# Kernel optimization log

Measured on AMD Instinct MI355X. Metric: run time of the kernel, lower is better.

## Reference

```python
import math
import jax, jax.numpy as jnp
import numpy as np

DIM = 128
NUM_PROJ = 256
B, H, SEQ = 2, 16, 4096


def _make_orthogonal_S(key):
    # Mirrors QJLWithOrthogonal.__init__: raw Gaussian, QR-orthogonalize each
    # dim-row chunk, scale by sqrt(dim).
    raw = jax.random.normal(key, (NUM_PROJ, DIM), dtype=jnp.float32)
    blocks = []
    for start in range(0, NUM_PROJ, DIM):
        block = raw[start:min(start + DIM, NUM_PROJ)]
        if block.shape[0] <= block.shape[1]:
            q, _ = jnp.linalg.qr(block.T)  # reduced QR of [dim, rows]
            blocks.append(q.T * np.float32(math.sqrt(DIM)))
        else:
            blocks.append(block)
    return jnp.concatenate(blocks, axis=0)[:NUM_PROJ]


def setup_inputs() -> dict:
    key = jax.random.key(0)
    kq, kk, ks = jax.random.split(key, 3)
    query = jax.random.normal(kq, (B, H, SEQ, DIM), dtype=jnp.float32)
    key_t = jax.random.normal(kk, (B, H, SEQ, DIM), dtype=jnp.float32)
    S = _make_orthogonal_S(ks)
    return {"query": query, "key": key_t, "S": S}


def reference(query, key, S):
    # quantize(key): sign of JL projection -> {-1, +1}, shape [B,H,S,m]
    z = jnp.sign(jnp.einsum('bhsd,md->bhsm', key, S))
    # estimate_inner_product(query, z): asymmetric estimator
    qp = jnp.einsum('bhsd,md->bhsm', query, S)
    scale = np.float32(math.sqrt(math.pi / 2) / NUM_PROJ)
    return scale * jnp.sum(qp * z, axis=-1)  # [B,H,S]
```

## Files before the change

kernel.cpp:

```cpp
#include <hip/hip_runtime.h>
#include <hip/hip_bf16.h>


#define DIM        128
#define NPROJ      256
#define TILE_T     32
#define NWG        4096
#define NBLK_P     256
#define TILES_PB   (NWG / NBLK_P)
#define LDS_STRIDE 136
#define TAU        6.0e-3f
#define SCALE      0.0048957583489668f

#define SHI_ELEMS  32768
#define TILE_ELEMS (TILE_T * LDS_STRIDE)
#define SMEM_BYTES ((2*SHI_ELEMS + 3*TILE_ELEMS) * 2 + 4 * TILE_T * 4)

typedef __attribute__((ext_vector_type(8))) short short8;
typedef __attribute__((ext_vector_type(4))) float f32x4;

static __device__ __forceinline__ unsigned short bf16_rne(float x){
    unsigned int u = __builtin_bit_cast(unsigned int, x);
    u += 0x7FFFu + ((u >> 16) & 1u);
    return (unsigned short)(u >> 16);
}

static __device__ __attribute__((noinline))
float ref_sign(const float* __restrict__ Kg, const float* __restrict__ S,
               int tok, int m){
    const float4* kr = (const float4*)(Kg + (size_t)tok * DIM);
    const float4* sr = (const float4*)(S  + (size_t)m   * DIM);
    float acc = 0.f;
#pragma unroll 4
    for (int d = 0; d < DIM/4; ++d){
        float4 k4 = kr[d];
        float4 s4 = sr[d];
        acc = __builtin_fmaf(k4.x, s4.x, acc);
        acc = __builtin_fmaf(k4.y, s4.y, acc);
        acc = __builtin_fmaf(k4.z, s4.z, acc);
        acc = __builtin_fmaf(k4.w, s4.w, acc);
    }
    return (acc > 0.f) ? 1.f : ((acc < 0.f) ? -1.f : 0.f);
}

__global__ void prep_s_kernel(const float* __restrict__ S,
                              unsigned short* __restrict__ shi,
                              unsigned short* __restrict__ slo){
    int t    = blockIdx.x * 256 + threadIdx.x;
    int lane = t & 63;
    int ms   = (t >> 6) & 3;
    int ks   = (t >> 8) & 3;
    int g    = (t >> 10) & 3;
    int m    = g*64 + ms*16 + (lane & 15);
    int d    = ks*32 + (lane >> 4)*8;
    const float4* p = (const float4*)(S + (size_t)m*DIM + d);
    float4 x0 = p[0], x1 = p[1];
    float xs[8] = {x0.x,x0.y,x0.z,x0.w, x1.x,x1.y,x1.z,x1.w};
    size_t base = ((size_t)t) * 8;
    unsigned long long h0=0,h1=0,l0=0,l1=0;
#pragma unroll
    for (int e = 0; e < 4; ++e){
        unsigned short hb = bf16_rne(xs[e]);
        float hf = __builtin_bit_cast(float, (unsigned int)hb << 16);
        h0 |= (unsigned long long)hb                    << (16*e);
        l0 |= (unsigned long long)bf16_rne(xs[e] - hf)  << (16*e);
    }
#pragma unroll
    for (int e = 0; e < 4; ++e){
        unsigned short hb = bf16_rne(xs[4+e]);
        float hf = __builtin_bit_cast(float, (unsigned int)hb << 16);
        h1 |= (unsigned long long)hb                      << (16*e);
        l1 |= (unsigned long long)bf16_rne(xs[4+e] - hf)  << (16*e);
    }
    *(unsigned long long*)(shi + base)     = h0;
    *(unsigned long long*)(shi + base + 4) = h1;
    *(unsigned long long*)(slo + base)     = l0;
    *(unsigned long long*)(slo + base + 4) = l1;
}


__global__ __launch_bounds__(256, 1)
void qjl_persistent(const float* __restrict__ Qg, const float* __restrict__ Kg,
                    const float* __restrict__ S,
                    const unsigned short* __restrict__ shi_tab,
                    const unsigned short* __restrict__ slo_tab,
                    float* __restrict__ out)
{
    extern __shared__ unsigned short smem_us[];
    unsigned short* s_hi = smem_us;
    unsigned short* s_lo = s_hi + SHI_ELEMS;
    unsigned short* khi  = s_lo + SHI_ELEMS;
    unsigned short* klo  = khi + TILE_ELEMS;
    unsigned short* qhi  = klo + TILE_ELEMS;
    float* red = (float*)(qhi + TILE_ELEMS);

    const int tid  = threadIdx.x;
    const int wave = tid >> 6;
    const int lane = tid & 63;
    const int l16  = lane & 15;
    const int quad = lane >> 4;

    {
        const short8* gh = (const short8*)shi_tab;
        const short8* gl = (const short8*)slo_tab;
        short8* lh = (short8*)s_hi;
        short8* ll = (short8*)s_lo;
#pragma unroll
        for (int j = 0; j < 16; ++j){
            int c = tid + j*256;
            lh[c] = gh[c];
            ll[c] = gl[c];
        }
    }

    float4 kv[4], qv[4];
    {
        const size_t t0 = (size_t)blockIdx.x * TILES_PB * TILE_T * DIM;
        const float4* ksrc = (const float4*)(Kg + t0);
        const float4* qsrc = (const float4*)(Qg + t0);
#pragma unroll
        for (int j = 0; j < 4; ++j){ kv[j] = ksrc[tid + j*256]; qv[j] = qsrc[tid + j*256]; }
    }

#pragma unroll 1
    for (int it = 0; it < TILES_PB; ++it){
        const int tok0 = (blockIdx.x * TILES_PB + it) * TILE_T;

#pragma unroll
        for (int j = 0; j < 4; ++j){
            int i   = tid + j*256;
            int row = i >> 5;
            int c   = i & 31;
            float kx[4] = {kv[j].x, kv[j].y, kv[j].z, kv[j].w};
            float qx[4] = {qv[j].x, qv[j].y, qv[j].z, qv[j].w};
            unsigned long long hp = 0, lp = 0, qp = 0;
#pragma unroll
            for (int e = 0; e < 4; ++e){
                unsigned short hb = bf16_rne(kx[e]);
                float hf = __builtin_bit_cast(float, (unsigned int)hb << 16);
                hp |= (unsigned long long)hb                   << (16*e);
                lp |= (unsigned long long)bf16_rne(kx[e] - hf) << (16*e);
                qp |= (unsigned long long)bf16_rne(qx[e])      << (16*e);
            }
            int base = row * LDS_STRIDE + c*4;
            *(unsigned long long*)(khi + base) = hp;
            *(unsigned long long*)(klo + base) = lp;
            *(unsigned long long*)(qhi + base) = qp;
        }
        __syncthreads();

        if (it + 1 < TILES_PB){
            const size_t tn = (size_t)(tok0 + TILE_T) * DIM;
            const float4* ksrc = (const float4*)(Kg + tn);
            const float4* qsrc = (const float4*)(Qg + tn);
#pragma unroll
            for (int j = 0; j < 4; ++j){ kv[j] = ksrc[tid + j*256]; qv[j] = qsrc[tid + j*256]; }
        }

        f32x4 accC[4][2];
        f32x4 accQ[4][2];
#pragma unroll
        for (int ms = 0; ms < 4; ++ms)
#pragma unroll
            for (int ts = 0; ts < 2; ++ts){
                accC[ms][ts] = (f32x4){0.f,0.f,0.f,0.f};
                accQ[ms][ts] = (f32x4){0.f,0.f,0.f,0.f};
            }

#pragma unroll
        for (int ks = 0; ks < 4; ++ks){
            short8 ah[4], al[4];
#pragma unroll
            for (int ms = 0; ms < 4; ++ms){
                int off = (((wave*4 + ks)*4 + ms)*64 + lane)*8;
                ah[ms] = *(const short8*)(s_hi + off);
                al[ms] = *(const short8*)(s_lo + off);
            }
#pragma unroll
            for (int ts = 0; ts < 2; ++ts){
                const int off = (ts*16 + l16) * LDS_STRIDE + ks*32 + quad*8;
                short8 bk = *(const short8*)(khi + off);
                short8 bl = *(const short8*)(klo + off);
                short8 bq = *(const short8*)(qhi + off);
#pragma unroll
                for (int ms = 0; ms < 4; ++ms){
                    accC[ms][ts] = __builtin_amdgcn_mfma_f32_16x16x32_bf16(ah[ms], bk, accC[ms][ts], 0,0,0);
                    accC[ms][ts] = __builtin_amdgcn_mfma_f32_16x16x32_bf16(al[ms], bk, accC[ms][ts], 0,0,0);
                    accC[ms][ts] = __builtin_amdgcn_mfma_f32_16x16x32_bf16(ah[ms], bl, accC[ms][ts], 0,0,0);
                    accQ[ms][ts] = __builtin_amdgcn_mfma_f32_16x16x32_bf16(ah[ms], bq, accQ[ms][ts], 0,0,0);
                }
            }
        }

        float part0 = 0.f, part1 = 0.f;
#pragma unroll
        for (int ts = 0; ts < 2; ++ts){
#pragma unroll
            for (int ms = 0; ms < 4; ++ms){
#pragma unroll
                for (int r = 0; r < 4; ++r){
                    float c = accC[ms][ts][r];
                    float s = (c >= 0.f) ? 1.f : -1.f;
                    if (__builtin_fabsf(c) < TAU)
                        s = ref_sign(Kg, S, tok0 + ts*16 + l16,
                                     wave*64 + ms*16 + quad*4 + r);
                    float sv = s * accQ[ms][ts][r];
                    if (ts) part1 += sv; else part0 += sv;
                }
            }
        }

        part0 += __shfl_xor(part0, 16, 64);
        part0 += __shfl_xor(part0, 32, 64);
        part1 += __shfl_xor(part1, 16, 64);
        part1 += __shfl_xor(part1, 32, 64);
        if (quad == 0){
            red[wave*TILE_T + l16]      = part0;
            red[wave*TILE_T + 16 + l16] = part1;
        }
        __syncthreads();
        if (tid < TILE_T)
            out[tok0 + tid] = SCALE * (red[0*TILE_T + tid] + red[1*TILE_T + tid] +
                                       red[2*TILE_T + tid] + red[3*TILE_T + tid]);
    }
}


template<bool USE_TAB>
static __device__ __forceinline__
void load_afrags(const unsigned short* __restrict__ shi_tab,
                 const unsigned short* __restrict__ slo_tab,
                 const float* __restrict__ S,
                 int wave, int ks, int l16, int quad, int lane,
                 short8 ah[4], short8 al[4]){
    if (USE_TAB){
#pragma unroll
        for (int ms = 0; ms < 4; ++ms){
            size_t off = ((size_t)((wave*4 + ks)*4 + ms)*64 + lane)*8;
            ah[ms] = *(const short8*)(shi_tab + off);
            al[ms] = *(const short8*)(slo_tab + off);
        }
    } else {
#pragma unroll
        for (int ms = 0; ms < 4; ++ms){
            const float4* p = (const float4*)(S + (size_t)(wave*64 + ms*16 + l16)*DIM
                                              + ks*32 + quad*8);
            float4 x0 = p[0], x1 = p[1];
            float xs[8] = {x0.x,x0.y,x0.z,x0.w, x1.x,x1.y,x1.z,x1.w};
            short8 h, l;
#pragma unroll
            for (int e = 0; e < 8; ++e){
                unsigned short hb = bf16_rne(xs[e]);
                float hf = __builtin_bit_cast(float, (unsigned int)hb << 16);
                h[e] = (short)hb;
                l[e] = (short)bf16_rne(xs[e] - hf);
            }
            ah[ms] = h;
            al[ms] = l;
        }
    }
}

template<bool USE_TAB>
__global__ __launch_bounds__(256, 4)
void qjl_kernel(const float* __restrict__ Qg, const float* __restrict__ Kg,
                const float* __restrict__ S,
                const unsigned short* __restrict__ shi_tab,
                const unsigned short* __restrict__ slo_tab,
                float* __restrict__ out)
{
    __shared__ unsigned short khi[TILE_T * LDS_STRIDE];
    __shared__ unsigned short klo[TILE_T * LDS_STRIDE];
    __shared__ unsigned short qhi[TILE_T * LDS_STRIDE];
    __shared__ float red[4][TILE_T];

    const int tid  = threadIdx.x;
    const int wave = tid >> 6;
    const int lane = tid & 63;
    const int l16  = lane & 15;
    const int quad = lane >> 4;
    const int tok0 = blockIdx.x * TILE_T;

    {
        const float4* ksrc = (const float4*)(Kg + (size_t)tok0 * DIM);
        const float4* qsrc = (const float4*)(Qg + (size_t)tok0 * DIM);
        float4 kv[4], qv[4];
#pragma unroll
        for (int j = 0; j < 4; ++j){ kv[j] = ksrc[tid + j*256]; qv[j] = qsrc[tid + j*256]; }
#pragma unroll
        for (int j = 0; j < 4; ++j){
            int i   = tid + j*256;
            int row = i >> 5;
            int c   = i & 31;
            float kx[4] = {kv[j].x, kv[j].y, kv[j].z, kv[j].w};
            float qx[4] = {qv[j].x, qv[j].y, qv[j].z, qv[j].w};
            unsigned long long hp = 0, lp = 0, qp = 0;
#pragma unroll
            for (int e = 0; e < 4; ++e){
                unsigned short hb = bf16_rne(kx[e]);
                float hf = __builtin_bit_cast(float, (unsigned int)hb << 16);
                hp |= (unsigned long long)hb                   << (16*e);
                lp |= (unsigned long long)bf16_rne(kx[e] - hf) << (16*e);
                qp |= (unsigned long long)bf16_rne(qx[e])      << (16*e);
            }
            int base = row * LDS_STRIDE + c*4;
            *(unsigned long long*)(khi + base) = hp;
            *(unsigned long long*)(klo + base) = lp;
            *(unsigned long long*)(qhi + base) = qp;
        }
    }
    __syncthreads();

    f32x4 accC[4][2];
    f32x4 accQ[4][2];
#pragma unroll
    for (int ms = 0; ms < 4; ++ms)
#pragma unroll
        for (int ts = 0; ts < 2; ++ts){
            accC[ms][ts] = (f32x4){0.f,0.f,0.f,0.f};
            accQ[ms][ts] = (f32x4){0.f,0.f,0.f,0.f};
        }

#pragma unroll
    for (int ks = 0; ks < 4; ++ks){
        short8 ah[4], al[4];
        load_afrags<USE_TAB>(shi_tab, slo_tab, S, wave, ks, l16, quad, lane, ah, al);
#pragma unroll
        for (int ts = 0; ts < 2; ++ts){
            const int off = (ts*16 + l16) * LDS_STRIDE + ks*32 + quad*8;
            short8 bk = *(const short8*)(khi + off);
            short8 bl = *(const short8*)(klo + off);
            short8 bq = *(const short8*)(qhi + off);
#pragma unroll
            for (int ms = 0; ms < 4; ++ms){
                accC[ms][ts] = __builtin_amdgcn_mfma_f32_16x16x32_bf16(ah[ms], bk, accC[ms][ts], 0,0,0);
                accC[ms][ts] = __builtin_amdgcn_mfma_f32_16x16x32_bf16(al[ms], bk, accC[ms][ts], 0,0,0);
                accC[ms][ts] = __builtin_amdgcn_mfma_f32_16x16x32_bf16(ah[ms], bl, accC[ms][ts], 0,0,0);
                accQ[ms][ts] = __builtin_amdgcn_mfma_f32_16x16x32_bf16(ah[ms], bq, accQ[ms][ts], 0,0,0);
            }
        }
    }

    float part0 = 0.f, part1 = 0.f;
#pragma unroll
    for (int ts = 0; ts < 2; ++ts){
#pragma unroll
        for (int ms = 0; ms < 4; ++ms){
#pragma unroll
            for (int r = 0; r < 4; ++r){
                float c = accC[ms][ts][r];
                float s = (c >= 0.f) ? 1.f : -1.f;
                if (__builtin_fabsf(c) < TAU)
                    s = ref_sign(Kg, S, tok0 + ts*16 + l16,
                                 wave*64 + ms*16 + quad*4 + r);
                float sv = s * accQ[ms][ts][r];
                if (ts) part1 += sv; else part0 += sv;
            }
        }
    }

    part0 += __shfl_xor(part0, 16, 64);
    part0 += __shfl_xor(part0, 32, 64);
    part1 += __shfl_xor(part1, 16, 64);
    part1 += __shfl_xor(part1, 32, 64);
    if (quad == 0){
        red[wave][l16]      = part0;
        red[wave][16 + l16] = part1;
    }
    __syncthreads();
    if (tid < TILE_T)
        out[tok0 + tid] = SCALE * (red[0][tid] + red[1][tid] + red[2][tid] + red[3][tid]);
}

extern "C" void kernel_launch(void* const* d_in, const int* in_sizes, int n_in,
                              void* d_out, int out_size, void* d_ws, size_t ws_size,
                              hipStream_t stream){
    const float* Qg = (const float*)d_in[0];
    const float* Kg = (const float*)d_in[1];
    const float* S  = (const float*)d_in[2];
    float* out = (float*)d_out;

    const size_t tab_elems = (size_t)NPROJ * DIM;
    const size_t need = 2 * tab_elems * sizeof(unsigned short);

    static int attr_ok = -1;
    if (attr_ok < 0){
        hipError_t e = hipFuncSetAttribute(
            reinterpret_cast<const void*>(&qjl_persistent),
            hipFuncAttributeMaxDynamicSharedMemorySize, SMEM_BYTES);
        attr_ok = (e == hipSuccess) ? 1 : 0;
    }

    if (d_ws && ws_size >= need){
        unsigned short* shi = (unsigned short*)d_ws;
        unsigned short* slo = shi + tab_elems;
        prep_s_kernel<<<16, 256, 0, stream>>>(S, shi, slo);
        if (attr_ok){
            qjl_persistent<<<NBLK_P, 256, SMEM_BYTES, stream>>>(Qg, Kg, S, shi, slo, out);
        } else {
            qjl_kernel<true><<<NWG, 256, 0, stream>>>(Qg, Kg, S, shi, slo, out);
        }
    } else {
        qjl_kernel<false><<<NWG, 256, 0, stream>>>(Qg, Kg, S, nullptr, nullptr, out);
    }
}
```

Measured before the change: 223.1 us.

## Hold projection fragments in registers and launch more smaller blocks

The persistent kernel staged the full bf16 hi/lo projection tables in about 140KB of LDS, allowing only one block per CU. The new kernel loads each wave's slice of the tables into registers once (32 short8 fragments per lane), keeps only the token tiles in LDS, and launches 1024 blocks of 4 tiles with a two-blocks-per-CU launch bound. The MFMA calls are also regrouped by operand so independent accumulators are issued back to back. This removes the per-iteration LDS reads of the A fragments and raises occupancy, at the cost of heavy VGPR pressure (128 registers for fragments) and a per-block table reload from global/L2.

```diff
diff --git a/kernel.cpp b/kernel.cpp
--- a/kernel.cpp
+++ b/kernel.cpp
@@ -6,15 +6,11 @@
 #define NPROJ      256
 #define TILE_T     32
 #define NWG        4096
-#define NBLK_P     256
-#define TILES_PB   (NWG / NBLK_P)
+#define NBLK_R     1024
+#define TPB        4
 #define LDS_STRIDE 136
 #define TAU        6.0e-3f
 #define SCALE      0.0048957583489668f
-
-#define SHI_ELEMS  32768
-#define TILE_ELEMS (TILE_T * LDS_STRIDE)
-#define SMEM_BYTES ((2*SHI_ELEMS + 3*TILE_ELEMS) * 2 + 4 * TILE_T * 4)
 
 typedef __attribute__((ext_vector_type(8))) short short8;
 typedef __attribute__((ext_vector_type(4))) float f32x4;
@@ -79,20 +75,17 @@
 }
 
 
-__global__ __launch_bounds__(256, 1)
-void qjl_persistent(const float* __restrict__ Qg, const float* __restrict__ Kg,
-                    const float* __restrict__ S,
-                    const unsigned short* __restrict__ shi_tab,
-                    const unsigned short* __restrict__ slo_tab,
-                    float* __restrict__ out)
+__global__ __launch_bounds__(256, 2)
+void qjl_reg(const float* __restrict__ Qg, const float* __restrict__ Kg,
+             const float* __restrict__ S,
+             const unsigned short* __restrict__ shi_tab,
+             const unsigned short* __restrict__ slo_tab,
+             float* __restrict__ out)
 {
-    extern __shared__ unsigned short smem_us[];
-    unsigned short* s_hi = smem_us;
-    unsigned short* s_lo = s_hi + SHI_ELEMS;
-    unsigned short* khi  = s_lo + SHI_ELEMS;
-    unsigned short* klo  = khi + TILE_ELEMS;
-    unsigned short* qhi  = klo + TILE_ELEMS;
-    float* red = (float*)(qhi + TILE_ELEMS);
+    __shared__ unsigned short khi[TILE_T * LDS_STRIDE];
+    __shared__ unsigned short klo[TILE_T * LDS_STRIDE];
+    __shared__ unsigned short qhi[TILE_T * LDS_STRIDE];
+    __shared__ float red[4][TILE_T];
 
     const int tid  = threadIdx.x;
     const int wave = tid >> 6;
@@ -100,22 +93,19 @@
     const int l16  = lane & 15;
     const int quad = lane >> 4;
 
-    {
-        const short8* gh = (const short8*)shi_tab;
-        const short8* gl = (const short8*)slo_tab;
-        short8* lh = (short8*)s_hi;
-        short8* ll = (short8*)s_lo;
-#pragma unroll
-        for (int j = 0; j < 16; ++j){
-            int c = tid + j*256;
-            lh[c] = gh[c];
-            ll[c] = gl[c];
-        }
-    }
+    short8 sh[4][4], sl[4][4];
+#pragma unroll
+    for (int ks = 0; ks < 4; ++ks)
+#pragma unroll
+        for (int ms = 0; ms < 4; ++ms){
+            size_t off = ((size_t)((wave*4 + ks)*4 + ms)*64 + lane)*8;
+            sh[ks][ms] = *(const short8*)(shi_tab + off);
+            sl[ks][ms] = *(const short8*)(slo_tab + off);
+        }
 
     float4 kv[4], qv[4];
     {
-        const size_t t0 = (size_t)blockIdx.x * TILES_PB * TILE_T * DIM;
+        const size_t t0 = (size_t)blockIdx.x * TPB * TILE_T * DIM;
         const float4* ksrc = (const float4*)(Kg + t0);
         const float4* qsrc = (const float4*)(Qg + t0);
 #pragma unroll
@@ -123,8 +113,8 @@
     }
 
 #pragma unroll 1
-    for (int it = 0; it < TILES_PB; ++it){
-        const int tok0 = (blockIdx.x * TILES_PB + it) * TILE_T;
+    for (int it = 0; it < TPB; ++it){
+        const int tok0 = (blockIdx.x * TPB + it) * TILE_T;
 
 #pragma unroll
         for (int j = 0; j < 4; ++j){
@@ -149,7 +139,7 @@
         }
         __syncthreads();
 
-        if (it + 1 < TILES_PB){
+        if (it + 1 < TPB){
             const size_t tn = (size_t)(tok0 + TILE_T) * DIM;
             const float4* ksrc = (const float4*)(Kg + tn);
             const float4* qsrc = (const float4*)(Qg + tn);
@@ -169,13 +159,6 @@
 
 #pragma unroll
         for (int ks = 0; ks < 4; ++ks){
-            short8 ah[4], al[4];
-#pragma unroll
-            for (int ms = 0; ms < 4; ++ms){
-                int off = (((wave*4 + ks)*4 + ms)*64 + lane)*8;
-                ah[ms] = *(const short8*)(s_hi + off);
-                al[ms] = *(const short8*)(s_lo + off);
-            }
 #pragma unroll
             for (int ts = 0; ts < 2; ++ts){
                 const int off = (ts*16 + l16) * LDS_STRIDE + ks*32 + quad*8;
@@ -183,12 +166,17 @@
                 short8 bl = *(const short8*)(klo + off);
                 short8 bq = *(const short8*)(qhi + off);
 #pragma unroll
-                for (int ms = 0; ms < 4; ++ms){
-                    accC[ms][ts] = __builtin_amdgcn_mfma_f32_16x16x32_bf16(ah[ms], bk, accC[ms][ts], 0,0,0);
-                    accC[ms][ts] = __builtin_amdgcn_mfma_f32_16x16x32_bf16(al[ms], bk, accC[ms][ts], 0,0,0);
-                    accC[ms][ts] = __builtin_amdgcn_mfma_f32_16x16x32_bf16(ah[ms], bl, accC[ms][ts], 0,0,0);
-                    accQ[ms][ts] = __builtin_amdgcn_mfma_f32_16x16x32_bf16(ah[ms], bq, accQ[ms][ts], 0,0,0);
-                }
+                for (int ms = 0; ms < 4; ++ms)
+                    accC[ms][ts] = __builtin_amdgcn_mfma_f32_16x16x32_bf16(sh[ks][ms], bk, accC[ms][ts], 0,0,0);
+#pragma unroll
+                for (int ms = 0; ms < 4; ++ms)
+                    accC[ms][ts] = __builtin_amdgcn_mfma_f32_16x16x32_bf16(sl[ks][ms], bk, accC[ms][ts], 0,0,0);
+#pragma unroll
+                for (int ms = 0; ms < 4; ++ms)
+                    accC[ms][ts] = __builtin_amdgcn_mfma_f32_16x16x32_bf16(sh[ks][ms], bl, accC[ms][ts], 0,0,0);
+#pragma unroll
+                for (int ms = 0; ms < 4; ++ms)
+                    accQ[ms][ts] = __builtin_amdgcn_mfma_f32_16x16x32_bf16(sh[ks][ms], bq, accQ[ms][ts], 0,0,0);
             }
         }
 
@@ -215,13 +203,12 @@
         part1 += __shfl_xor(part1, 16, 64);
         part1 += __shfl_xor(part1, 32, 64);
         if (quad == 0){
-            red[wave*TILE_T + l16]      = part0;
-            red[wave*TILE_T + 16 + l16] = part1;
+            red[wave][l16]      = part0;
+            red[wave][16 + l16] = part1;
         }
         __syncthreads();
         if (tid < TILE_T)
-            out[tok0 + tid] = SCALE * (red[0*TILE_T + tid] + red[1*TILE_T + tid] +
-                                       red[2*TILE_T + tid] + red[3*TILE_T + tid]);
+            out[tok0 + tid] = SCALE * (red[0][tid] + red[1][tid] + red[2][tid] + red[3][tid]);
     }
 }
 
@@ -383,23 +370,11 @@
     const size_t tab_elems = (size_t)NPROJ * DIM;
     const size_t need = 2 * tab_elems * sizeof(unsigned short);
 
-    static int attr_ok = -1;
-    if (attr_ok < 0){
-        hipError_t e = hipFuncSetAttribute(
-            reinterpret_cast<const void*>(&qjl_persistent),
-            hipFuncAttributeMaxDynamicSharedMemorySize, SMEM_BYTES);
-        attr_ok = (e == hipSuccess) ? 1 : 0;
-    }
-
     if (d_ws && ws_size >= need){
         unsigned short* shi = (unsigned short*)d_ws;
         unsigned short* slo = shi + tab_elems;
         prep_s_kernel<<<16, 256, 0, stream>>>(S, shi, slo);
-        if (attr_ok){
-            qjl_persistent<<<NBLK_P, 256, SMEM_BYTES, stream>>>(Qg, Kg, S, shi, slo, out);
-        } else {
-            qjl_kernel<true><<<NWG, 256, 0, stream>>>(Qg, Kg, S, shi, slo, out);
-        }
+        qjl_reg<<<NBLK_R, 256, 0, stream>>>(Qg, Kg, S, shi, slo, out);
     } else {
         qjl_kernel<false><<<NWG, 256, 0, stream>>>(Qg, Kg, S, nullptr, nullptr, out);
     }
```

Result: slower. 238.3 us (+6.8%).
